# Optimization experiments

Hardware: AMD Instinct MI355X
Metric: run time of the kernel (lower is better)

The kernel has to match this reference:

```python
import jax, jax.numpy as jnp
import numpy as np

B, T, IN, H, OUT = 4096, 512, 4, 64, 1


def setup_inputs() -> dict:
    key = jax.random.key(0)
    ks = jax.random.split(key, 12)
    s_in = 1.0 / np.sqrt(H)
    u = lambda k, shape: jax.random.uniform(k, shape, jnp.float32, -s_in, s_in)
    return {
        "x": jax.random.normal(ks[0], (B, T, IN), jnp.float32),
        "W_ih0": u(ks[1], (4 * H, IN)),
        "W_hh0": u(ks[2], (4 * H, H)),
        "b_ih0": u(ks[3], (4 * H,)),
        "b_hh0": u(ks[4], (4 * H,)),
        "W_ih1": u(ks[5], (4 * H, H)),
        "W_hh1": u(ks[6], (4 * H, H)),
        "b_ih1": u(ks[7], (4 * H,)),
        "b_hh1": u(ks[8], (4 * H,)),
        "W_fc": u(ks[9], (OUT, H)),
        "b_fc": u(ks[10], (OUT,)),
    }


def _lstm_layer(x_seq, W_ih, W_hh, b_ih, b_hh):
    # x_seq: [B, T, D]. PyTorch gate order: i, f, g, o.
    # Precompute input projection for all timesteps (one big GEMM).
    x_proj = jnp.einsum("btd,gd->btg", x_seq, W_ih) + b_ih + b_hh  # [B, T, 4H]
    x_proj = jnp.swapaxes(x_proj, 0, 1)  # [T, B, 4H]
    Bsz = x_seq.shape[0]
    h0 = jnp.zeros((Bsz, W_hh.shape[1]), x_seq.dtype)
    c0 = jnp.zeros_like(h0)

    def step(carry, xp):
        h, c = carry
        gates = xp + h @ W_hh.T  # [B, 4H]
        i, f, g, o = jnp.split(gates, 4, axis=-1)
        i = jax.nn.sigmoid(i)
        f = jax.nn.sigmoid(f)
        g = jnp.tanh(g)
        o = jax.nn.sigmoid(o)
        c_new = f * c + i * g
        h_new = o * jnp.tanh(c_new)
        return (h_new, c_new), h_new

    (hT, cT), h_seq = jax.lax.scan(step, (h0, c0), x_proj)
    return jnp.swapaxes(h_seq, 0, 1), hT  # [B, T, H], [B, H]


def reference(x, W_ih0, W_hh0, b_ih0, b_hh0, W_ih1, W_hh1, b_ih1, b_hh1, W_fc, b_fc):
    h1_seq, _ = _lstm_layer(x, W_ih0, W_hh0, b_ih0, b_hh0)
    _, h2_last = _lstm_layer(h1_seq, W_ih1, W_hh1, b_ih1, b_hh1)
    return h2_last @ W_fc.T + b_fc  # [B, 1]
```

## Files before the change

### kernel.cpp

```cpp
#include <hip/hip_runtime.h>

#define TSEQ 512
#define NTH  512

typedef __attribute__((ext_vector_type(8))) _Float16 half8;
typedef __attribute__((ext_vector_type(4))) float f32x4;
typedef __attribute__((ext_vector_type(4))) unsigned int u32x4;

__device__ __forceinline__ unsigned packF16x2(float a, float b) {
    _Float16 ha = (_Float16)a, hb = (_Float16)b;
    unsigned short ua = __builtin_bit_cast(unsigned short, ha);
    unsigned short ub = __builtin_bit_cast(unsigned short, hb);
    return (unsigned)ua | ((unsigned)ub << 16);
}
__device__ __forceinline__ half8 packA16s(const float w8[8], float s) {
    u32x4 W = { packF16x2(w8[0]*s, w8[1]*s), packF16x2(w8[2]*s, w8[3]*s),
                packF16x2(w8[4]*s, w8[5]*s), packF16x2(w8[6]*s, w8[7]*s) };
    return __builtin_bit_cast(half8, W);
}

#define MFMA(a, b, c) __builtin_amdgcn_mfma_f32_16x16x32_f16((a), (b), (c), 0, 0, 0)
#define LD128H(p) __builtin_bit_cast(half8, *(const u32x4*)(p))

__device__ __forceinline__ float act_fused(float ai, float af, float ag, float ao, float* c) {
    const float L2E2 = 2.88539008177792681472f;
    float ei = __builtin_amdgcn_exp2f(ai);
    float ef = __builtin_amdgcn_exp2f(af);
    float eg = __builtin_amdgcn_exp2f(ag);
    float eo = __builtin_amdgcn_exp2f(ao);
    float sf = __builtin_amdgcn_rcpf(1.0f + ef);
    float ig = (eg - 1.0f) * __builtin_amdgcn_rcpf((1.0f + ei) * (eg + 1.0f));
    float cn = fmaf(*c, sf, ig);
    *c = cn;
    float ec = __builtin_amdgcn_exp2f(cn * L2E2);
    return (ec - 1.0f) * __builtin_amdgcn_rcpf((1.0f + eo) * (ec + 1.0f));
}

__global__ __launch_bounds__(NTH, 1)
void lstm2_mfma(const float* __restrict__ x,
                const float* __restrict__ W_ih0, const float* __restrict__ W_hh0,
                const float* __restrict__ b_ih0, const float* __restrict__ b_hh0,
                const float* __restrict__ W_ih1, const float* __restrict__ W_hh1,
                const float* __restrict__ b_ih1, const float* __restrict__ b_hh1,
                const float* __restrict__ W_fc,  const float* __restrict__ b_fc,
                float* __restrict__ out)
{
    const int tid  = threadIdx.x;
    const int lane = tid & 63;
    const int wv   = tid >> 6;
    const int rl   = lane & 15;
    const int g    = lane >> 4;
    const int b0   = blockIdx.x * 16;

    const float NL2E = -1.44269504088896340736f;
    const float PL2E2 = 2.88539008177792681472f;

    __shared__ unsigned h0P0[512], h0P1[512];
    __shared__ unsigned h1P0[512], h1P1[512];
    __shared__ float fcl[64 * 17];

    for (int i2 = tid; i2 < 512; i2 += NTH) {
        h0P0[i2] = 0u; h0P1[i2] = 0u; h1P0[i2] = 0u; h1P1[i2] = 0u;
    }
    __syncthreads();

    const int offL = rl*32 + (((g + rl) & 7) << 2);
    const int offH = rl*32 + (((4 + g + rl) & 7) << 2);
    const int q0w  = 8*((wv & 3)) + 2*g;
    const int woff = rl*32 + ((((q0w >> 2) + rl) & 7) << 2) + (q0w & 3);

    if (wv < 4) {
        const int w = wv;
        half8 A0[4][2];
        half8 Ax[4];
        f32x4 bias4[4];
        #pragma unroll
        for (int G = 0; G < 4; ++G) {
            const float sc = (G == 2) ? PL2E2 : NL2E;
            const int row = 64*G + 16*w + rl;
            #pragma unroll
            for (int s = 0; s < 2; ++s) {
                float w8[8];
                const float* src = W_hh0 + row*64 + s*32 + g*8;
                #pragma unroll
                for (int e = 0; e < 8; ++e) w8[e] = src[e];
                A0[G][s] = packA16s(w8, sc);
            }
            {
                u32x4 ax = {0u, 0u, 0u, 0u};
                if (g == 0) {
                    ax.x = packF16x2(W_ih0[row*4+0]*sc, W_ih0[row*4+1]*sc);
                    ax.y = packF16x2(W_ih0[row*4+2]*sc, W_ih0[row*4+3]*sc);
                }
                Ax[G] = __builtin_bit_cast(half8, ax);
            }
            const int rb = 64*G + 16*w + 4*g;
            bias4[G].x = (b_ih0[rb+0] + b_hh0[rb+0]) * sc;
            bias4[G].y = (b_ih0[rb+1] + b_hh0[rb+1]) * sc;
            bias4[G].z = (b_ih0[rb+2] + b_hh0[rb+2]) * sc;
            bias4[G].w = (b_ih0[rb+3] + b_hh0[rb+3]) * sc;
        }
        float cst[4] = {0.f, 0.f, 0.f, 0.f};

        f32x4 xf = *(const f32x4*)(x + ((size_t)(b0 + rl) * TSEQ) * 4);
        unsigned bx0 = packF16x2(xf.x, xf.y);
        unsigned bx1 = packF16x2(xf.z, xf.w);

        auto body0 = [&](const unsigned* rP, unsigned* wP, int i) {
            if (i + 1 < TSEQ)
                xf = *(const f32x4*)(x + ((size_t)(b0 + rl) * TSEQ + (i + 1)) * 4);

            half8 B0 = LD128H(rP + offL);
            half8 B1 = LD128H(rP + offH);
            u32x4 tx = {0u, 0u, 0u, 0u};
            if (g == 0) { tx.x = bx0; tx.y = bx1; }
            half8 Bx = __builtin_bit_cast(half8, tx);

            f32x4 acc[4];
            __builtin_amdgcn_s_setprio(1);
            #pragma unroll
            for (int G = 0; G < 4; ++G) acc[G] = MFMA(Ax[G], Bx, bias4[G]);
            #pragma unroll
            for (int G = 0; G < 4; ++G) acc[G] = MFMA(A0[G][0], B0, acc[G]);
            #pragma unroll
            for (int G = 0; G < 4; ++G) acc[G] = MFMA(A0[G][1], B1, acc[G]);
            __builtin_amdgcn_s_setprio(0);

            float hv[4];
            #pragma unroll
            for (int j = 0; j < 4; ++j)
                hv[j] = act_fused(acc[0][j], acc[1][j], acc[2][j], acc[3][j], &cst[j]);

            bx0 = packF16x2(xf.x, xf.y);
            bx1 = packF16x2(xf.z, xf.w);

            *(uint2*)(wP + woff) = make_uint2(packF16x2(hv[0], hv[1]),
                                              packF16x2(hv[2], hv[3]));
        };

        for (int ii = 0; ii < 256; ++ii) {
            body0(h0P0, h0P1, 2*ii);     __syncthreads();
            body0(h0P1, h0P0, 2*ii + 1); __syncthreads();
        }
        __syncthreads();
        __syncthreads();
    } else {
        const int w = wv - 4;
        half8 A1[4][4];
        f32x4 bias4[4];
        #pragma unroll
        for (int G = 0; G < 4; ++G) {
            const float sc = (G == 2) ? PL2E2 : NL2E;
            const int row = 64*G + 16*w + rl;
            #pragma unroll
            for (int s = 0; s < 4; ++s) {
                float w8[8];
                const float* src = (s < 2) ? (W_ih1 + row*64 + s*32 + g*8)
                                           : (W_hh1 + row*64 + (s-2)*32 + g*8);
                #pragma unroll
                for (int e = 0; e < 8; ++e) w8[e] = src[e];
                A1[G][s] = packA16s(w8, sc);
            }
            const int rb = 64*G + 16*w + 4*g;
            bias4[G].x = (b_ih1[rb+0] + b_hh1[rb+0]) * sc;
            bias4[G].y = (b_ih1[rb+1] + b_hh1[rb+1]) * sc;
            bias4[G].z = (b_ih1[rb+2] + b_hh1[rb+2]) * sc;
            bias4[G].w = (b_ih1[rb+3] + b_hh1[rb+3]) * sc;
        }
        float cst[4] = {0.f, 0.f, 0.f, 0.f};
        const int u0 = 16*w + 4*g;

        half8 pB0 = {}, pB1 = {};

        auto body1 = [&](const unsigned* r1P,
                         unsigned* wP,
                         const unsigned* n0P,
                         bool wrFC) {
            half8 B2 = LD128H(r1P + offL);
            half8 B3 = LD128H(r1P + offH);

            f32x4 acc[4];
            __builtin_amdgcn_s_setprio(1);
            #pragma unroll
            for (int G = 0; G < 4; ++G) acc[G] = MFMA(A1[G][0], pB0, bias4[G]);
            #pragma unroll
            for (int G = 0; G < 4; ++G) acc[G] = MFMA(A1[G][1], pB1, acc[G]);
            #pragma unroll
            for (int G = 0; G < 4; ++G) acc[G] = MFMA(A1[G][2], B2, acc[G]);
            #pragma unroll
            for (int G = 0; G < 4; ++G) acc[G] = MFMA(A1[G][3], B3, acc[G]);
            __builtin_amdgcn_s_setprio(0);

            pB0 = LD128H(n0P + offL);
            pB1 = LD128H(n0P + offH);

            float hv[4];
            #pragma unroll
            for (int j = 0; j < 4; ++j)
                hv[j] = act_fused(acc[0][j], acc[1][j], acc[2][j], acc[3][j], &cst[j]);
            *(uint2*)(wP + woff) = make_uint2(packF16x2(hv[0], hv[1]),
                                              packF16x2(hv[2], hv[3]));
            if (wrFC) {
                #pragma unroll
                for (int j = 0; j < 4; ++j) fcl[(u0 + j)*17 + rl] = hv[j];
            }
        };

        __syncthreads();
        pB0 = LD128H(h0P1 + offL);
        pB1 = LD128H(h0P1 + offH);
        __syncthreads();
        for (int ii = 0; ii < 256; ++ii) {
            body1(h1P0, h1P1, h0P0, false);     __syncthreads();
            body1(h1P1, h1P0, h0P1, ii == 255); __syncthreads();
        }
    }

    if (tid < 16) {
        float acc = b_fc[0];
        #pragma unroll 16
        for (int u = 0; u < 64; ++u) acc += fcl[u*17 + tid] * W_fc[u];
        out[b0 + tid] = acc;
    }
}

extern "C" void kernel_launch(void* const* d_in, const int* in_sizes, int n_in,
                              void* d_out, int out_size, void* d_ws, size_t ws_size,
                              hipStream_t stream) {
    const float* x     = (const float*)d_in[0];
    const float* W_ih0 = (const float*)d_in[1];
    const float* W_hh0 = (const float*)d_in[2];
    const float* b_ih0 = (const float*)d_in[3];
    const float* b_hh0 = (const float*)d_in[4];
    const float* W_ih1 = (const float*)d_in[5];
    const float* W_hh1 = (const float*)d_in[6];
    const float* b_ih1 = (const float*)d_in[7];
    const float* b_hh1 = (const float*)d_in[8];
    const float* W_fc  = (const float*)d_in[9];
    const float* b_fc  = (const float*)d_in[10];
    float* out = (float*)d_out;

    dim3 grid(4096 / 16), block(NTH);
    hipLaunchKernelGGL(lstm2_mfma, grid, block, 0, stream,
                       x, W_ih0, W_hh0, b_ih0, b_hh0,
                       W_ih1, W_hh1, b_ih1, b_hh1, W_fc, b_fc, out);
}
```

Baseline: 341.7 us.

## Replace block barriers with LDS producer/consumer flags between LSTM layer waves

Replaces the per-timestep __syncthreads lockstep between the layer-0 and layer-1 wave groups with per-slot atomic producer/consumer counters in shared memory. Layer-0 h states go into a 4-deep ring buffer and layer-1 h into a 2-deep ring, so layer 0 can run up to a few steps ahead of layer 1 and the two layers no longer wait on each other every step. The cost is spin-waiting on LDS atomics with acquire/release ordering, which adds polling overhead and a risk of subtle ordering bugs.

```diff
diff --git a/kernel.cpp b/kernel.cpp
--- a/kernel.cpp
+++ b/kernel.cpp
@@ -52,22 +52,32 @@
     const int g    = lane >> 4;
     const int b0   = blockIdx.x * 16;
 
-    const float NL2E = -1.44269504088896340736f;
-    const float PL2E2 = 2.88539008177792681472f;
-
-    __shared__ unsigned h0P0[512], h0P1[512];
-    __shared__ unsigned h1P0[512], h1P1[512];
+    const float NL2E  = -1.44269504088896340736f;
+    const float PL2E2 =  2.88539008177792681472f;
+
+    __shared__ unsigned h0S[4][512];
+    __shared__ unsigned h1S[2][512];
     __shared__ float fcl[64 * 17];
-
-    for (int i2 = tid; i2 < 512; i2 += NTH) {
-        h0P0[i2] = 0u; h0P1[i2] = 0u; h1P0[i2] = 0u; h1P1[i2] = 0u;
-    }
+    __shared__ unsigned prodH0[4], consH0[4], prodH1[2], consH1[2];
+
+    for (int i2 = tid; i2 < 4*512; i2 += NTH) ((unsigned*)h0S)[i2] = 0u;
+    for (int i2 = tid; i2 < 2*512; i2 += NTH) ((unsigned*)h1S)[i2] = 0u;
+    if (tid < 4) { prodH0[tid] = 0u; consH0[tid] = 0u; }
+    if (tid < 2) { prodH1[tid] = 0u; consH1[tid] = 0u; }
     __syncthreads();
 
     const int offL = rl*32 + (((g + rl) & 7) << 2);
     const int offH = rl*32 + (((4 + g + rl) & 7) << 2);
     const int q0w  = 8*((wv & 3)) + 2*g;
     const int woff = rl*32 + ((((q0w >> 2) + rl) & 7) << 2) + (q0w & 3);
+
+    auto waitge = [&](unsigned* p, unsigned tgt) {
+        while (__hip_atomic_load(p, __ATOMIC_ACQUIRE, __HIP_MEMORY_SCOPE_WORKGROUP) < tgt) {}
+    };
+    auto signal = [&](unsigned* p) {
+        if (lane == 0)
+            __hip_atomic_fetch_add(p, 1u, __ATOMIC_RELEASE, __HIP_MEMORY_SCOPE_WORKGROUP);
+    };
 
     if (wv < 4) {
         const int w = wv;
@@ -106,10 +116,16 @@
         unsigned bx0 = packF16x2(xf.x, xf.y);
         unsigned bx1 = packF16x2(xf.z, xf.w);
 
-        auto body0 = [&](const unsigned* rP, unsigned* wP, int i) {
-            if (i + 1 < TSEQ)
-                xf = *(const f32x4*)(x + ((size_t)(b0 + rl) * TSEQ + (i + 1)) * 4);
-
+        for (int t = 0; t < TSEQ; ++t) {
+            const int rs = (t - 1) & 3;
+            const int ws = t & 3;
+            if (t >= 1) waitge(&prodH0[rs], 4u * (unsigned)(((t - 1) >> 2) + 1));
+            if (t >= 4) waitge(&consH0[ws], 8u * (unsigned)(t >> 2));
+
+            if (t + 1 < TSEQ)
+                xf = *(const f32x4*)(x + ((size_t)(b0 + rl) * TSEQ + (t + 1)) * 4);
+
+            const unsigned* rP = h0S[rs];
             half8 B0 = LD128H(rP + offL);
             half8 B1 = LD128H(rP + offH);
             u32x4 tx = {0u, 0u, 0u, 0u};
@@ -126,6 +142,8 @@
             for (int G = 0; G < 4; ++G) acc[G] = MFMA(A0[G][1], B1, acc[G]);
             __builtin_amdgcn_s_setprio(0);
 
+            if (t >= 1) signal(&consH0[rs]);
+
             float hv[4];
             #pragma unroll
             for (int j = 0; j < 4; ++j)
@@ -134,16 +152,10 @@
             bx0 = packF16x2(xf.x, xf.y);
             bx1 = packF16x2(xf.z, xf.w);
 
-            *(uint2*)(wP + woff) = make_uint2(packF16x2(hv[0], hv[1]),
-                                              packF16x2(hv[2], hv[3]));
-        };
-
-        for (int ii = 0; ii < 256; ++ii) {
-            body0(h0P0, h0P1, 2*ii);     __syncthreads();
-            body0(h0P1, h0P0, 2*ii + 1); __syncthreads();
-        }
-        __syncthreads();
-        __syncthreads();
+            *(uint2*)(h0S[ws] + woff) = make_uint2(packF16x2(hv[0], hv[1]),
+                                                   packF16x2(hv[2], hv[3]));
+            signal(&prodH0[ws]);
+        }
     } else {
         const int w = wv - 4;
         half8 A1[4][4];
@@ -170,14 +182,18 @@
         float cst[4] = {0.f, 0.f, 0.f, 0.f};
         const int u0 = 16*w + 4*g;
 
-        half8 pB0 = {}, pB1 = {};
-
-        auto body1 = [&](const unsigned* r1P,
-                         unsigned* wP,
-                         const unsigned* n0P,
-                         bool wrFC) {
-            half8 B2 = LD128H(r1P + offL);
-            half8 B3 = LD128H(r1P + offH);
+        for (int t = 0; t < TSEQ; ++t) {
+            const int h0s = t & 3;
+            const int h1r = (t - 1) & 1;
+            const int h1w = t & 1;
+
+            waitge(&prodH0[h0s], 4u * (unsigned)((t >> 2) + 1));
+            half8 pB0 = LD128H(h0S[h0s] + offL);
+            half8 pB1 = LD128H(h0S[h0s] + offH);
+            if (t >= 1) waitge(&prodH1[h1r], 4u * (unsigned)((t + 1) >> 1));
+            half8 B2 = LD128H(h1S[h1r] + offL);
+            half8 B3 = LD128H(h1S[h1r] + offH);
+            if (t >= 2) waitge(&consH1[h1w], 4u * (unsigned)((t + 1) >> 1));
 
             f32x4 acc[4];
             __builtin_amdgcn_s_setprio(1);
@@ -191,30 +207,24 @@
             for (int G = 0; G < 4; ++G) acc[G] = MFMA(A1[G][3], B3, acc[G]);
             __builtin_amdgcn_s_setprio(0);
 
-            pB0 = LD128H(n0P + offL);
-            pB1 = LD128H(n0P + offH);
+            signal(&consH0[h0s]);
+            signal(&consH1[h1r]);
 
             float hv[4];
             #pragma unroll
             for (int j = 0; j < 4; ++j)
                 hv[j] = act_fused(acc[0][j], acc[1][j], acc[2][j], acc[3][j], &cst[j]);
-            *(uint2*)(wP + woff) = make_uint2(packF16x2(hv[0], hv[1]),
-                                              packF16x2(hv[2], hv[3]));
-            if (wrFC) {
+            *(uint2*)(h1S[h1w] + woff) = make_uint2(packF16x2(hv[0], hv[1]),
+                                                    packF16x2(hv[2], hv[3]));
+            signal(&prodH1[h1w]);
+
+            if (t == TSEQ - 1) {
                 #pragma unroll
                 for (int j = 0; j < 4; ++j) fcl[(u0 + j)*17 + rl] = hv[j];
             }
-        };
-
-        __syncthreads();
-        pB0 = LD128H(h0P1 + offL);
-        pB1 = LD128H(h0P1 + offH);
-        __syncthreads();
-        for (int ii = 0; ii < 256; ++ii) {
-            body1(h1P0, h1P1, h0P0, false);     __syncthreads();
-            body1(h1P1, h1P0, h0P1, ii == 255); __syncthreads();
         }
     }
+    __syncthreads();
 
     if (tid < 16) {
         float acc = b_fc[0];
```

Result: slower. 499.6 us (+46.2%).
